# Kernel tuning notes

Measured on AMD Instinct MI355X. Metric: run time of the kernel, lower is better.

Reference implementation:

```python
import jax, jax.numpy as jnp
import numpy as np

HIDDEN = 1024
NUM_HEAD = 16
HEAD_DIM = HIDDEN // NUM_HEAD
VOCAB = 32000
MAX_LEN = 1024
EMBED = 512
BATCH = 4
SEQ = MAX_LEN  # mask broadcasting requires seq == max_len


def setup_inputs() -> dict:
    key = jax.random.key(0)
    ks = jax.random.split(key, 12)
    std = 0.02
    inp = {
        'input_ids': jax.random.randint(ks[0], (BATCH, SEQ), 0, VOCAB),
        'W_word': jax.random.normal(ks[1], (VOCAB, EMBED), jnp.float32) * std,
        'W_pos': jax.random.normal(ks[2], (MAX_LEN, EMBED), jnp.float32) * std,
        'Wq': jax.random.normal(ks[3], (HIDDEN, HIDDEN), jnp.float32) * std,
        'Wk': jax.random.normal(ks[4], (HIDDEN, HIDDEN), jnp.float32) * std,
        'Wv': jax.random.normal(ks[5], (HIDDEN, HIDDEN), jnp.float32) * std,
        'Wo': jax.random.normal(ks[6], (HIDDEN, HIDDEN), jnp.float32) * std,
        'W1': jax.random.normal(ks[7], (4 * HIDDEN, HIDDEN), jnp.float32) * std,
        'W2': jax.random.normal(ks[8], (HIDDEN, 4 * HIDDEN), jnp.float32) * std,
        'W_eh': jax.random.normal(ks[9], (HIDDEN, EMBED), jnp.float32) * std,
        'W_he': jax.random.normal(ks[10], (EMBED, HIDDEN), jnp.float32) * std,
        'W_lm': jax.random.normal(ks[11], (VOCAB, EMBED), jnp.float32) * std,
    }
    return inp


def reference(input_ids, W_word, W_pos, Wq, Wk, Wv, Wo, W1, W2, W_eh, W_he, W_lm):
    B, S = input_ids.shape
    # embeddings
    h = W_word[input_ids] + W_pos[jnp.arange(S)][None, :, :]  # [B,S,E]
    h = h @ W_eh.T  # embed -> hidden, [B,S,H]
    residual = h
    # QKV projections (Linear with weight [out,in]: y = x @ W.T)
    q = (h @ Wq.T).reshape(B, S, NUM_HEAD, HEAD_DIM).transpose(0, 2, 1, 3)
    k = (h @ Wk.T).reshape(B, S, NUM_HEAD, HEAD_DIM).transpose(0, 2, 1, 3)
    v = (h @ Wv.T).reshape(B, S, NUM_HEAD, HEAD_DIM).transpose(0, 2, 1, 3)
    # note: original scales by sqrt(hidden_size), NOT sqrt(head_dim)
    scores = jnp.einsum('bhqd,bhkd->bhqk', q, k) / jnp.sqrt(jnp.float32(HIDDEN))
    mask = jnp.tril(jnp.ones((S, S), dtype=bool))[None, None]
    scores = jnp.where(mask, scores, jnp.finfo(jnp.float32).min)
    attn = jax.nn.softmax(scores.astype(jnp.float32), axis=-1)
    out = jnp.einsum('bhqk,bhkd->bhqd', attn, v)
    out = out.transpose(0, 2, 1, 3).reshape(B, S, HIDDEN)
    h = residual + out @ Wo.T
    # MLP
    residual = h
    x = jax.nn.relu(h @ W1.T)
    h = residual + x @ W2.T
    # hidden -> embed, lm head
    h = h @ W_he.T
    logits = h @ W_lm.T  # [B,S,VOCAB]
    return logits
```

## Files before the change

kernel.cpp:

```cpp
#include <hip/hip_runtime.h>
#include <hip/hip_bf16.h>

#define HIDDEN 1024
#define NHEAD 16
#define HDIM 64
#define VOCAB 32000
#define SEQLEN 1024
#define EMBED 512
#define BATCH 4
#define ROWS (BATCH*SEQLEN)

typedef __bf16 bf16x8 __attribute__((ext_vector_type(8)));
typedef float f32x4 __attribute__((ext_vector_type(4)));
typedef unsigned short u16;

#define MFMA(a_, b_, c_) __builtin_amdgcn_mfma_f32_16x16x32_bf16(a_, b_, c_, 0, 0, 0)

#define VMCNT4 asm volatile("s_waitcnt vmcnt(4)" ::: "memory")
#define VMCNT0 asm volatile("s_waitcnt vmcnt(0)" ::: "memory")
#define LGKM0  asm volatile("s_waitcnt lgkmcnt(0)" ::: "memory")
#define CFENCE asm volatile("" ::: "memory")
#define SBAR   __builtin_amdgcn_s_barrier()
#define SCHEDB __builtin_amdgcn_sched_barrier(0)

__device__ __forceinline__ u16 f2bf(float f) {
  unsigned u = __builtin_bit_cast(unsigned, f);
  u = u + 0x7FFFu + ((u >> 16) & 1u);
  return (u16)(u >> 16);
}

#define GLDS(g_, l_) __builtin_amdgcn_global_load_lds( \
    (const __attribute__((address_space(1))) void*)(g_), \
    (__attribute__((address_space(3))) void*)(l_), 16, 0, 0)

struct Prep {
  const float* src[8]; u16* dst[8];
  const float* wlm; u16* wlm_dst;
  const int* ids; const float* wword; const float* wpos; u16* h0b;
};
__global__ void prep_kernel(Prep pp) {
  int b = blockIdx.x;
  if (b < 13312) {
    int seg, off;
    if (b < 4096)        { seg = b >> 10; off = b & 1023; }
    else if (b < 8192)   { seg = 4; off = b - 4096; }
    else if (b < 12288)  { seg = 5; off = b - 8192; }
    else if (b < 12800)  { seg = 6; off = b - 12288; }
    else                 { seg = 7; off = b - 12800; }
    size_t i = ((size_t)off * 256 + threadIdx.x) * 4;
    float4 v = *(const float4*)(pp.src[seg] + i);
    unsigned a = f2bf(v.x) | ((unsigned)f2bf(v.y) << 16);
    unsigned d = f2bf(v.z) | ((unsigned)f2bf(v.w) << 16);
    *(uint2*)(pp.dst[seg] + i) = make_uint2(a, d);
  } else if (b < 29312) {
    if (!pp.wlm_dst) return;
    int off = b - 13312;
    size_t i = ((size_t)off * 256 + threadIdx.x) * 4;
    float4 v = *(const float4*)(pp.wlm + i);
    unsigned a = f2bf(v.x) | ((unsigned)f2bf(v.y) << 16);
    unsigned d = f2bf(v.z) | ((unsigned)f2bf(v.w) << 16);
    *(uint2*)(pp.wlm_dst + i) = make_uint2(a, d);
  } else {
    int off = b - 29312;
    int row = off * 2 + (threadIdx.x >> 7);
    int e = (threadIdx.x & 127) * 4;
    int s = row & (SEQLEN - 1);
    int id = pp.ids[row];
    float4 a = *(const float4*)(pp.wword + (size_t)id * EMBED + e);
    float4 c = *(const float4*)(pp.wpos + (size_t)s * EMBED + e);
    unsigned lo = f2bf(a.x + c.x) | ((unsigned)f2bf(a.y + c.y) << 16);
    unsigned hi = f2bf(a.z + c.z) | ((unsigned)f2bf(a.w + c.w) << 16);
    *(uint2*)(pp.h0b + (size_t)row * EMBED + e) = make_uint2(lo, hi);
  }
}

template<int EPI, bool WF32, bool WB16, bool BF32, bool SWZ, bool NT = false>
__global__ __launch_bounds__(256, 2) void gemm128(
    const u16* __restrict__ A, const u16* __restrict__ Bb,
    const float* __restrict__ Bf,
    float* __restrict__ C, u16* __restrict__ Cb,
    const float* __restrict__ R, int K, int ldc)
{
  __shared__ u16 As[2][128 * 64];
  __shared__ u16 Bs[2][128 * 64];
  int tid = threadIdx.x;
  int lane = tid & 63, wave = tid >> 6;
  int wr = wave >> 1, wc = wave & 1;
  int cl = lane & 15, gp = (lane >> 4) & 3;

  int bx = blockIdx.x, by = blockIdx.y;
  if (SWZ) {
    int nwg = gridDim.x * gridDim.y;
    int flat = by * gridDim.x + bx;
    int cpx = nwg >> 3;
    int swz = (flat & 7) * cpx + (flat >> 3);
    bx = swz % gridDim.x; by = swz / gridDim.x;
  }
  int m0 = bx * 128, n0 = by * 128;

  int srow8 = lane >> 3;
  int scol = (((lane & 7) - srow8) & 7) * 8;
  int pos0 = ((gp + cl) & 7) * 8;
  int pos1 = ((gp + cl + 4) & 7) * 8;

  f32x4 acc[4][4] = {};
  int nk = K >> 6;

  #pragma unroll
  for (int i = 0; i < 4; ++i) {
    int c = i * 4 + wave;
    GLDS(A + (size_t)(m0 + c * 8 + srow8) * K + scol, &As[0][c * 512]);
  }
  if (!BF32) {
    #pragma unroll
    for (int i = 0; i < 4; ++i) {
      int c = i * 4 + wave;
      GLDS(Bb + (size_t)(n0 + c * 8 + srow8) * K + scol, &Bs[0][c * 512]);
    }
  } else {
    #pragma unroll
    for (int it = 0; it < 4; ++it) {
      int idx = it * 256 + tid;
      int row = idx >> 3, p = idx & 7;
      int gc = (p - row) & 7;
      const float* src = Bf + (size_t)(n0 + row) * K + gc * 8;
      float4 v0 = *(const float4*)src, v1 = *(const float4*)(src + 4);
      union { bf16x8 v; u16 s[8]; } u;
      u.s[0]=f2bf(v0.x); u.s[1]=f2bf(v0.y); u.s[2]=f2bf(v0.z); u.s[3]=f2bf(v0.w);
      u.s[4]=f2bf(v1.x); u.s[5]=f2bf(v1.y); u.s[6]=f2bf(v1.z); u.s[7]=f2bf(v1.w);
      *(bf16x8*)&Bs[0][row * 64 + p * 8] = u.v;
    }
  }

  for (int kt = 0; kt < nk; ++kt) {
    int buf = kt & 1;
    int kb = (kt + 1) << 6;
    bool more = kt + 1 < nk;

    if (more) {
      #pragma unroll
      for (int i = 0; i < 4; ++i) {
        int c = i * 4 + wave;
        GLDS(A + (size_t)(m0 + c * 8 + srow8) * K + kb + scol, &As[buf ^ 1][c * 512]);
      }
    }
    if (BF32) { VMCNT0; } else if (more) { VMCNT4; } else { VMCNT0; }
    SCHEDB;
    SBAR;
    CFENCE; SCHEDB;

    bf16x8 af[4][2], bfv[4][2];
    #pragma unroll
    for (int n = 0; n < 4; ++n) {
      int r = (wc * 64 + n * 16 + cl) * 64;
      bfv[n][0] = *(const bf16x8*)&Bs[buf][r + pos0];
      bfv[n][1] = *(const bf16x8*)&Bs[buf][r + pos1];
    }
    #pragma unroll
    for (int m = 0; m < 4; ++m) {
      int r = (wr * 64 + m * 16 + cl) * 64;
      af[m][0] = *(const bf16x8*)&As[buf][r + pos0];
      af[m][1] = *(const bf16x8*)&As[buf][r + pos1];
    }

    __builtin_amdgcn_s_setprio(1);
    #pragma unroll
    for (int m = 0; m < 2; ++m)
      #pragma unroll
      for (int n = 0; n < 4; ++n)
        #pragma unroll
        for (int ks = 0; ks < 2; ++ks)
          acc[m][n] = MFMA(af[m][ks], bfv[n][ks], acc[m][n]);
    __builtin_amdgcn_s_setprio(0);

    if (more) {
      if (!BF32) {
        #pragma unroll
        for (int i = 0; i < 4; ++i) {
          int c = i * 4 + wave;
          GLDS(Bb + (size_t)(n0 + c * 8 + srow8) * K + kb + scol, &Bs[buf ^ 1][c * 512]);
        }
      } else {
        #pragma unroll
        for (int it = 0; it < 4; ++it) {
          int idx = it * 256 + tid;
          int row = idx >> 3, p = idx & 7;
          int gc = (p - row) & 7;
          const float* src = Bf + (size_t)(n0 + row) * K + kb + gc * 8;
          float4 v0 = *(const float4*)src, v1 = *(const float4*)(src + 4);
          union { bf16x8 v; u16 s[8]; } u;
          u.s[0]=f2bf(v0.x); u.s[1]=f2bf(v0.y); u.s[2]=f2bf(v0.z); u.s[3]=f2bf(v0.w);
          u.s[4]=f2bf(v1.x); u.s[5]=f2bf(v1.y); u.s[6]=f2bf(v1.z); u.s[7]=f2bf(v1.w);
          *(bf16x8*)&Bs[buf ^ 1][row * 64 + p * 8] = u.v;
        }
      }
    }

    __builtin_amdgcn_s_setprio(1);
    #pragma unroll
    for (int n = 0; n < 4; ++n)
      #pragma unroll
      for (int ks = 0; ks < 2; ++ks)
        acc[2][n] = MFMA(af[2][ks], bfv[n][ks], acc[2][n]);
    __builtin_amdgcn_s_setprio(0);

    LGKM0;
    SCHEDB;
    SBAR;
    CFENCE; SCHEDB;

    __builtin_amdgcn_s_setprio(1);
    #pragma unroll
    for (int n = 0; n < 4; ++n)
      #pragma unroll
      for (int ks = 0; ks < 2; ++ks)
        acc[3][n] = MFMA(af[3][ks], bfv[n][ks], acc[3][n]);
    __builtin_amdgcn_s_setprio(0);
  }

  int r0 = gp * 4;
  #pragma unroll
  for (int m = 0; m < 4; ++m) {
    #pragma unroll
    for (int n = 0; n < 4; ++n) {
      int col = n0 + wc * 64 + n * 16 + cl;
      #pragma unroll
      for (int j = 0; j < 4; ++j) {
        int row = m0 + wr * 64 + m * 16 + r0 + j;
        float v = acc[m][n][j];
        if (EPI == 1) v += R[(size_t)row * ldc + col];
        if (EPI == 2) v = fmaxf(v, 0.f);
        if (WF32) {
          if (NT) __builtin_nontemporal_store(v, &C[(size_t)row * ldc + col]);
          else C[(size_t)row * ldc + col] = v;
        }
        if (WB16) Cb[(size_t)row * ldc + col] = f2bf(v);
      }
    }
  }
}

template<int EPI, bool WF32, bool WB16, bool SWZ, bool NT = false>
__global__ __launch_bounds__(512) void gemm256(
    const u16* __restrict__ A, const u16* __restrict__ B,
    float* __restrict__ C, u16* __restrict__ Cb,
    const float* __restrict__ R, int K, int ldc)
{
  __shared__ __align__(16) u16 smem[4][256 * 64];
  int tid = threadIdx.x;
  int lane = tid & 63, wave = tid >> 6;
  int wr = wave >> 2, wc = wave & 3;
  int cl = lane & 15, gp = (lane >> 4) & 3;

  int bx = blockIdx.x, by = blockIdx.y;
  if (SWZ) {
    int nwg = gridDim.x * gridDim.y;
    int flat = by * gridDim.x + bx;
    int cpx = nwg >> 3;
    int swz = (flat & 7) * cpx + (flat >> 3);
    bx = swz % gridDim.x; by = swz / gridDim.x;
  }
  int m0 = bx * 256, n0 = by * 256;

  int srow8 = lane >> 3;
  int scol = (((lane & 7) - srow8) & 7) * 8;
  int pos0 = ((gp + cl) & 7) * 8;
  int pos1 = ((gp + cl + 4) & 7) * 8;

  f32x4 acc[8][4] = {};
  int nk = K >> 6;

  #pragma unroll
  for (int i = 0; i < 4; ++i) {
    int c = i * 8 + wave;
    GLDS(A + (size_t)(m0 + c * 8 + srow8) * K + scol, &smem[0][c * 512]);
  }
  #pragma unroll
  for (int i = 0; i < 4; ++i) {
    int c = i * 8 + wave;
    GLDS(B + (size_t)(n0 + c * 8 + srow8) * K + scol, &smem[2][c * 512]);
  }

  for (int kt = 0; kt < nk; ++kt) {
    int buf = kt & 1;
    int kb = (kt + 1) << 6;
    bool more = kt + 1 < nk;

    if (more) {
      #pragma unroll
      for (int i = 0; i < 4; ++i) {
        int c = i * 8 + wave;
        GLDS(A + (size_t)(m0 + c * 8 + srow8) * K + kb + scol, &smem[buf ^ 1][c * 512]);
      }
      VMCNT4;
    } else {
      VMCNT0;
    }
    SCHEDB;
    SBAR;
    CFENCE; SCHEDB;

    bf16x8 af0[4][2], af1[4][2], bf0[2][2], bf1[2][2];
    #pragma unroll
    for (int n = 0; n < 2; ++n) {
      int r = (wc * 64 + n * 16 + cl) * 64;
      bf0[n][0] = *(const bf16x8*)&smem[2 + buf][r + pos0];
      bf0[n][1] = *(const bf16x8*)&smem[2 + buf][r + pos1];
    }
    #pragma unroll
    for (int m = 0; m < 4; ++m) {
      int r = (wr * 128 + m * 16 + cl) * 64;
      af0[m][0] = *(const bf16x8*)&smem[buf][r + pos0];
      af0[m][1] = *(const bf16x8*)&smem[buf][r + pos1];
    }
    #pragma unroll
    for (int n = 0; n < 2; ++n) {
      int r = (wc * 64 + (n + 2) * 16 + cl) * 64;
      bf1[n][0] = *(const bf16x8*)&smem[2 + buf][r + pos0];
      bf1[n][1] = *(const bf16x8*)&smem[2 + buf][r + pos1];
    }
    #pragma unroll
    for (int m = 0; m < 4; ++m) {
      int r = (wr * 128 + (m + 4) * 16 + cl) * 64;
      af1[m][0] = *(const bf16x8*)&smem[buf][r + pos0];
      af1[m][1] = *(const bf16x8*)&smem[buf][r + pos1];
    }

    __builtin_amdgcn_s_setprio(1);
    #pragma unroll
    for (int m = 0; m < 4; ++m)
      #pragma unroll
      for (int n = 0; n < 2; ++n)
        #pragma unroll
        for (int ks = 0; ks < 2; ++ks)
          acc[m][n] = MFMA(af0[m][ks], bf0[n][ks], acc[m][n]);
    __builtin_amdgcn_s_setprio(0);

    if (more) {
      #pragma unroll
      for (int i = 0; i < 4; ++i) {
        int c = i * 8 + wave;
        GLDS(B + (size_t)(n0 + c * 8 + srow8) * K + kb + scol, &smem[2 + (buf ^ 1)][c * 512]);
      }
    }

    __builtin_amdgcn_s_setprio(1);
    #pragma unroll
    for (int m = 0; m < 4; ++m)
      #pragma unroll
      for (int n = 0; n < 2; ++n)
        #pragma unroll
        for (int ks = 0; ks < 2; ++ks)
          acc[m][n + 2] = MFMA(af0[m][ks], bf1[n][ks], acc[m][n + 2]);
    __builtin_amdgcn_s_setprio(0);

    LGKM0;
    SCHEDB;
    SBAR;
    CFENCE; SCHEDB;

    __builtin_amdgcn_s_setprio(1);
    #pragma unroll
    for (int m = 0; m < 4; ++m)
      #pragma unroll
      for (int n = 0; n < 2; ++n)
        #pragma unroll
        for (int ks = 0; ks < 2; ++ks)
          acc[m + 4][n] = MFMA(af1[m][ks], bf0[n][ks], acc[m + 4][n]);
    #pragma unroll
    for (int m = 0; m < 4; ++m)
      #pragma unroll
      for (int n = 0; n < 2; ++n)
        #pragma unroll
        for (int ks = 0; ks < 2; ++ks)
          acc[m + 4][n + 2] = MFMA(af1[m][ks], bf1[n][ks], acc[m + 4][n + 2]);
    __builtin_amdgcn_s_setprio(0);
  }

  if (WF32 && !WB16) {
    float* Cst = (float*)&smem[0][0];
    __syncthreads();
    #pragma unroll
    for (int g = 0; g < 4; ++g) {
      if ((g >> 1) == wr) {
        #pragma unroll
        for (int k = 0; k < 4; ++k) {
          int ar = (g & 1) * 4 + k;
          int rl = ar * 16 + gp * 4 - (g & 1) * 64;
          #pragma unroll
          for (int n = 0; n < 4; ++n) {
            int col = wc * 64 + n * 16 + cl;
            #pragma unroll
            for (int j = 0; j < 4; ++j)
              Cst[(rl + j) * 260 + col] = acc[ar][n][j];
          }
        }
      }
      __syncthreads();
      #pragma unroll
      for (int p = 0; p < 8; ++p) {
        int r = p * 8 + wave;
        int c4 = lane * 4;
        int grow = m0 + g * 64 + r;
        f32x4 v = *(f32x4*)&Cst[r * 260 + c4];
        if (EPI == 1) {
          f32x4 rv = *(const f32x4*)&R[(size_t)grow * ldc + n0 + c4];
          v = v + rv;
        }
        if (EPI == 2) {
          #pragma unroll
          for (int j = 0; j < 4; ++j) v[j] = fmaxf(v[j], 0.f);
        }
        if (NT) __builtin_nontemporal_store(v, (f32x4*)&C[(size_t)grow * ldc + n0 + c4]);
        else *(f32x4*)&C[(size_t)grow * ldc + n0 + c4] = v;
      }
      __syncthreads();
    }
  } else {
    int r0 = gp * 4;
    #pragma unroll
    for (int m = 0; m < 8; ++m) {
      #pragma unroll
      for (int n = 0; n < 4; ++n) {
        int col = n0 + wc * 64 + n * 16 + cl;
        #pragma unroll
        for (int j = 0; j < 4; ++j) {
          int row = m0 + wr * 128 + m * 16 + r0 + j;
          float v = acc[m][n][j];
          if (EPI == 1) v += R[(size_t)row * ldc + col];
          if (EPI == 2) v = fmaxf(v, 0.f);
          if (WF32) C[(size_t)row * ldc + col] = v;
          if (WB16) Cb[(size_t)row * ldc + col] = f2bf(v);
        }
      }
    }
  }
}

#define LSTR 72
__global__ __launch_bounds__(256) void attn_kernel(const u16* __restrict__ qkv,
                                                   u16* __restrict__ outb) {
  __shared__ u16 Ksm[2][64 * 64];
  __shared__ u16 Vsm[2][64 * LSTR];
  __shared__ u16 Psm[64 * LSTR];
  int qb = blockIdx.x, h = blockIdx.y, b = blockIdx.z;
  int tid = threadIdx.x;
  int lane = tid & 63, wave = tid >> 6;
  int cl = lane & 15, gp = lane >> 4;
  int srow8 = lane >> 3;
  int gsrc = (((lane & 7) - srow8) & 7) * 8;

  const u16* base = qkv + (size_t)b * SEQLEN * (3 * HIDDEN);

  int qrow_a = qb * 64 + wave * 16 + cl;
  const u16* qp = base + (size_t)qrow_a * (3 * HIDDEN) + h * HDIM;
  bf16x8 qf0 = *(const bf16x8*)(qp + gp * 8);
  bf16x8 qf1 = *(const bf16x8*)(qp + 32 + gp * 8);

  ushort4 vr[4];

  auto stageK = [&](int t, int bb) {
    #pragma unroll
    for (int i = 0; i < 2; ++i) {
      int c = wave * 2 + i;
      int row = c * 8 + srow8;
      GLDS(base + (size_t)(t * 64 + row) * (3 * HIDDEN) + HIDDEN + h * HDIM + gsrc,
           &Ksm[bb][c * 512]);
    }
  };
  auto loadV = [&](int t) {
    #pragma unroll
    for (int it = 0; it < 4; ++it) {
      int idx = it * 256 + tid;
      int row = idx >> 4, c4 = (idx & 15) * 4;
      vr[it] = *(const ushort4*)(base + (size_t)(t * 64 + row) * (3 * HIDDEN) +
                                 2 * HIDDEN + h * HDIM + c4);
    }
  };
  auto writeV = [&](int bb) {
    #pragma unroll
    for (int it = 0; it < 4; ++it) {
      int idx = it * 256 + tid;
      int row = idx >> 4, c4 = (idx & 15) * 4;
      Vsm[bb][(c4 + 0) * LSTR + row] = vr[it].x;
      Vsm[bb][(c4 + 1) * LSTR + row] = vr[it].y;
      Vsm[bb][(c4 + 2) * LSTR + row] = vr[it].z;
      Vsm[bb][(c4 + 3) * LSTR + row] = vr[it].w;
    }
  };

  stageK(0, 0);
  loadV(0);
  writeV(0);
  __syncthreads();

  float mrow[4], lrow[4];
  f32x4 oacc[4] = {};
  #pragma unroll
  for (int j = 0; j < 4; ++j) { mrow[j] = -INFINITY; lrow[j] = 0.f; }

  for (int t = 0; t <= qb; ++t) {
    int buf = t & 1;
    bool more = t < qb;
    if (more) { stageK(t + 1, buf ^ 1); loadV(t + 1); }

    f32x4 sfr[4];
    __builtin_amdgcn_s_setprio(1);
    #pragma unroll
    for (int n = 0; n < 4; ++n) {
      f32x4 z = {};
      bf16x8 kf0 = *(const bf16x8*)&Ksm[buf][(n * 16 + cl) * 64 + ((gp + cl) & 7) * 8];
      bf16x8 kf1 = *(const bf16x8*)&Ksm[buf][(n * 16 + cl) * 64 + ((gp + cl + 4) & 7) * 8];
      z = MFMA(qf0, kf0, z);
      z = MFMA(qf1, kf1, z);
      sfr[n] = z;
    }
    __builtin_amdgcn_s_setprio(0);

    #pragma unroll
    for (int n = 0; n < 4; ++n)
      #pragma unroll
      for (int j = 0; j < 4; ++j) {
        int qg = qb * 64 + wave * 16 + gp * 4 + j;
        int kg = t * 64 + n * 16 + cl;
        float sv = sfr[n][j] * 0.03125f;
        sfr[n][j] = (kg <= qg) ? sv : -1e30f;
      }
    float so[4];
    #pragma unroll
    for (int j = 0; j < 4; ++j) {
      float tm = fmaxf(fmaxf(sfr[0][j], sfr[1][j]), fmaxf(sfr[2][j], sfr[3][j]));
      tm = fmaxf(tm, __shfl_xor(tm, 1));
      tm = fmaxf(tm, __shfl_xor(tm, 2));
      tm = fmaxf(tm, __shfl_xor(tm, 4));
      tm = fmaxf(tm, __shfl_xor(tm, 8));
      float mn = fmaxf(mrow[j], tm);
      so[j] = __expf(mrow[j] - mn);
      mrow[j] = mn;
      float ts = 0.f;
      #pragma unroll
      for (int n = 0; n < 4; ++n) {
        float p = __expf(sfr[n][j] - mn);
        sfr[n][j] = p;
        ts += p;
      }
      ts += __shfl_xor(ts, 1); ts += __shfl_xor(ts, 2);
      ts += __shfl_xor(ts, 4); ts += __shfl_xor(ts, 8);
      lrow[j] = lrow[j] * so[j] + ts;
    }
    #pragma unroll
    for (int n = 0; n < 4; ++n)
      #pragma unroll
      for (int j = 0; j < 4; ++j)
        oacc[n][j] *= so[j];

    if (more) writeV(buf ^ 1);

    #pragma unroll
    for (int n = 0; n < 4; ++n)
      #pragma unroll
      for (int j = 0; j < 4; ++j)
        Psm[(wave * 16 + gp * 4 + j) * LSTR + n * 16 + cl] = f2bf(sfr[n][j]);
    __builtin_amdgcn_sched_barrier(0);

    bf16x8 pa0 = *(const bf16x8*)&Psm[(wave * 16 + cl) * LSTR + gp * 8];
    bf16x8 pa1 = *(const bf16x8*)&Psm[(wave * 16 + cl) * LSTR + 32 + gp * 8];
    __builtin_amdgcn_s_setprio(1);
    #pragma unroll
    for (int n = 0; n < 4; ++n) {
      bf16x8 vb0 = *(const bf16x8*)&Vsm[buf][(n * 16 + cl) * LSTR + gp * 8];
      bf16x8 vb1 = *(const bf16x8*)&Vsm[buf][(n * 16 + cl) * LSTR + 32 + gp * 8];
      oacc[n] = MFMA(pa0, vb0, oacc[n]);
      oacc[n] = MFMA(pa1, vb1, oacc[n]);
    }
    __builtin_amdgcn_s_setprio(0);

    __syncthreads();
  }

  #pragma unroll
  for (int n = 0; n < 4; ++n)
    #pragma unroll
    for (int j = 0; j < 4; ++j) {
      int qg = qb * 64 + wave * 16 + gp * 4 + j;
      int d = n * 16 + cl;
      outb[(size_t)(b * SEQLEN + qg) * HIDDEN + h * HDIM + d] = f2bf(oacc[n][j] / lrow[j]);
    }
}

extern "C" void kernel_launch(void* const* d_in, const int* in_sizes, int n_in,
                              void* d_out, int out_size, void* d_ws, size_t ws_size,
                              hipStream_t stream) {
  const int*   ids    = (const int*)d_in[0];
  const float* W_word = (const float*)d_in[1];
  const float* W_pos  = (const float*)d_in[2];
  const float* Wq     = (const float*)d_in[3];
  const float* Wk     = (const float*)d_in[4];
  const float* Wv     = (const float*)d_in[5];
  const float* Wo     = (const float*)d_in[6];
  const float* W1     = (const float*)d_in[7];
  const float* W2     = (const float*)d_in[8];
  const float* W_eh   = (const float*)d_in[9];
  const float* W_he   = (const float*)d_in[10];
  const float* W_lm   = (const float*)d_in[11];
  float* out = (float*)d_out;
  char*  ob  = (char*)d_out;
  char*  wb  = (char*)d_ws;

  const size_t MB = 1024 * 1024;
  float* h1    = (float*)(ob + 0 * MB);
  float* h2    = (float*)(ob + 16 * MB);
  u16*   h0b   = (u16*)(ob + 32 * MB);
  u16*   h1b   = (u16*)(ob + 36 * MB);
  u16*   qkvb  = (u16*)(ob + 44 * MB);
  u16*   attnb = (u16*)(ob + 68 * MB);
  u16*   h2b   = (u16*)(ob + 76 * MB);
  u16*   xb    = (u16*)(ob + 84 * MB);
  u16*   h3b   = (u16*)(ob + 116 * MB);
  u16*   Wqkv_b= (u16*)(ob + 124 * MB);
  u16*   Wo_b  = (u16*)(ob + 130 * MB);
  u16*   W1_b  = (u16*)(ob + 132 * MB);
  u16*   W2_b  = (u16*)(ob + 140 * MB);
  u16*   Weh_b = (u16*)(ob + 148 * MB);
  u16*   Whe_b = (u16*)(ob + 149 * MB);
  u16*   he_b  = (u16*)(wb + 0);
  u16*   Wlm_b = (u16*)(wb + 4 * MB);
  bool big_ws = ws_size >= 36 * MB;

  Prep pp;
  pp.src[0] = Wq;  pp.dst[0] = Wqkv_b + 0 * 1024 * 1024;
  pp.src[1] = Wk;  pp.dst[1] = Wqkv_b + 1 * 1024 * 1024;
  pp.src[2] = Wv;  pp.dst[2] = Wqkv_b + 2 * 1024 * 1024;
  pp.src[3] = Wo;  pp.dst[3] = Wo_b;
  pp.src[4] = W1;  pp.dst[4] = W1_b;
  pp.src[5] = W2;  pp.dst[5] = W2_b;
  pp.src[6] = W_eh; pp.dst[6] = Weh_b;
  pp.src[7] = W_he; pp.dst[7] = Whe_b;
  pp.wlm = W_lm; pp.wlm_dst = big_ws ? Wlm_b : nullptr;
  pp.ids = ids; pp.wword = W_word; pp.wpos = W_pos; pp.h0b = h0b;
  prep_kernel<<<dim3(31360), 256, 0, stream>>>(pp);

  gemm128<0, true, true, false, false><<<dim3(32, 8), 256, 0, stream>>>(
      h0b, Weh_b, nullptr, h1, h1b, nullptr, 512, HIDDEN);
  gemm128<0, false, true, false, false><<<dim3(32, 24), 256, 0, stream>>>(
      h1b, Wqkv_b, nullptr, nullptr, qkvb, nullptr, 1024, 3 * HIDDEN);
  attn_kernel<<<dim3(16, 16, 4), 256, 0, stream>>>(qkvb, attnb);
  gemm128<1, true, true, false, false><<<dim3(32, 8), 256, 0, stream>>>(
      attnb, Wo_b, nullptr, h2, h2b, h1, 1024, HIDDEN);
  gemm256<2, false, true, false><<<dim3(16, 16), 512, 0, stream>>>(
      h2b, W1_b, nullptr, xb, nullptr, 1024, 4 * HIDDEN);
  gemm128<1, false, true, false, false><<<dim3(32, 8), 256, 0, stream>>>(
      xb, W2_b, nullptr, nullptr, h3b, h2, 4096, HIDDEN);
  gemm128<0, false, true, false, false><<<dim3(32, 4), 256, 0, stream>>>(
      h3b, Whe_b, nullptr, nullptr, he_b, nullptr, 1024, EMBED);
  if (big_ws)
    gemm256<0, true, false, true, true><<<dim3(16, 125), 512, 0, stream>>>(
        he_b, Wlm_b, out, nullptr, nullptr, 512, VOCAB);
  else
    gemm128<0, true, false, true, true, true><<<dim3(32, 250), 256, 0, stream>>>(
        he_b, nullptr, W_lm, out, nullptr, nullptr, 512, VOCAB);
}
```

Measured before the change: 495.3 us.

## Pair causal attention blocks, use bf16 residuals, and templatize GEMM tile width

Attention now has each workgroup handle query block i and 15-i, which evens out work under the causal mask, halves the grid, and shares K/V staging between the two blocks. Residual adds read bf16 copies instead of fp32 h1/h2, so the fp32 writes and reads of those buffers are dropped. A BN template lets the small W_he GEMM use 64-wide tiles and double its grid, and a coalesced LDS-staged epilogue is added for fp32-only outputs. Rounding the residuals to bf16 lowers precision, and the pairing raises register pressure in the attention kernel.

Result: faster. 416.0 us (-16.0%).

```diff
diff --git a/kernel.cpp b/kernel.cpp
--- a/kernel.cpp
+++ b/kernel.cpp
@@ -27,6 +27,10 @@
   unsigned u = __builtin_bit_cast(unsigned, f);
   u = u + 0x7FFFu + ((u >> 16) & 1u);
   return (u16)(u >> 16);
+}
+__device__ __forceinline__ float bf2f(u16 s) {
+  unsigned u = (unsigned)s << 16;
+  return __builtin_bit_cast(float, u);
 }
 
 #define GLDS(g_, l_) __builtin_amdgcn_global_load_lds( \
@@ -74,15 +78,21 @@
   }
 }
 
-template<int EPI, bool WF32, bool WB16, bool BF32, bool SWZ, bool NT = false>
+template<int EPI, bool WF32, bool WB16, bool BF32, bool SWZ, bool NT, int BN>
 __global__ __launch_bounds__(256, 2) void gemm128(
     const u16* __restrict__ A, const u16* __restrict__ Bb,
     const float* __restrict__ Bf,
     float* __restrict__ C, u16* __restrict__ Cb,
-    const float* __restrict__ R, int K, int ldc)
+    const u16* __restrict__ R, int K, int ldc)
 {
-  __shared__ u16 As[2][128 * 64];
-  __shared__ u16 Bs[2][128 * 64];
+  constexpr int NF  = BN / 32;
+  constexpr int BCH = BN / 32;
+  __shared__ __align__(16) u16 smem[16384 + 2 * BN * 64];
+  u16* As0 = &smem[0];
+  u16* As1 = &smem[8192];
+  u16* Bs0 = &smem[16384];
+  u16* Bs1 = &smem[16384 + BN * 64];
+
   int tid = threadIdx.x;
   int lane = tid & 63, wave = tid >> 6;
   int wr = wave >> 1, wc = wave & 1;
@@ -96,30 +106,30 @@
     int swz = (flat & 7) * cpx + (flat >> 3);
     bx = swz % gridDim.x; by = swz / gridDim.x;
   }
-  int m0 = bx * 128, n0 = by * 128;
+  int m0 = bx * 128, n0 = by * BN;
 
   int srow8 = lane >> 3;
   int scol = (((lane & 7) - srow8) & 7) * 8;
   int pos0 = ((gp + cl) & 7) * 8;
   int pos1 = ((gp + cl + 4) & 7) * 8;
 
-  f32x4 acc[4][4] = {};
+  f32x4 acc[4][NF] = {};
   int nk = K >> 6;
 
   #pragma unroll
   for (int i = 0; i < 4; ++i) {
     int c = i * 4 + wave;
-    GLDS(A + (size_t)(m0 + c * 8 + srow8) * K + scol, &As[0][c * 512]);
+    GLDS(A + (size_t)(m0 + c * 8 + srow8) * K + scol, As0 + c * 512);
   }
   if (!BF32) {
     #pragma unroll
-    for (int i = 0; i < 4; ++i) {
+    for (int i = 0; i < BCH; ++i) {
       int c = i * 4 + wave;
-      GLDS(Bb + (size_t)(n0 + c * 8 + srow8) * K + scol, &Bs[0][c * 512]);
+      GLDS(Bb + (size_t)(n0 + c * 8 + srow8) * K + scol, Bs0 + c * 512);
     }
   } else {
     #pragma unroll
-    for (int it = 0; it < 4; ++it) {
+    for (int it = 0; it < BN / 32; ++it) {
       int idx = it * 256 + tid;
       int row = idx >> 3, p = idx & 7;
       int gc = (p - row) & 7;
@@ -128,12 +138,16 @@
       union { bf16x8 v; u16 s[8]; } u;
       u.s[0]=f2bf(v0.x); u.s[1]=f2bf(v0.y); u.s[2]=f2bf(v0.z); u.s[3]=f2bf(v0.w);
       u.s[4]=f2bf(v1.x); u.s[5]=f2bf(v1.y); u.s[6]=f2bf(v1.z); u.s[7]=f2bf(v1.w);
-      *(bf16x8*)&Bs[0][row * 64 + p * 8] = u.v;
+      *(bf16x8*)&Bs0[row * 64 + p * 8] = u.v;
     }
   }
 
   for (int kt = 0; kt < nk; ++kt) {
     int buf = kt & 1;
+    u16* Asb = buf ? As1 : As0;
+    u16* Bsb = buf ? Bs1 : Bs0;
+    u16* Asn = buf ? As0 : As1;
+    u16* Bsn = buf ? Bs0 : Bs1;
     int kb = (kt + 1) << 6;
     bool more = kt + 1 < nk;
 
@@ -141,7 +155,7 @@
       #pragma unroll
       for (int i = 0; i < 4; ++i) {
         int c = i * 4 + wave;
-        GLDS(A + (size_t)(m0 + c * 8 + srow8) * K + kb + scol, &As[buf ^ 1][c * 512]);
+        GLDS(A + (size_t)(m0 + c * 8 + srow8) * K + kb + scol, Asn + c * 512);
       }
     }
     if (BF32) { VMCNT0; } else if (more) { VMCNT4; } else { VMCNT0; }
@@ -149,25 +163,25 @@
     SBAR;
     CFENCE; SCHEDB;
 
-    bf16x8 af[4][2], bfv[4][2];
-    #pragma unroll
-    for (int n = 0; n < 4; ++n) {
-      int r = (wc * 64 + n * 16 + cl) * 64;
-      bfv[n][0] = *(const bf16x8*)&Bs[buf][r + pos0];
-      bfv[n][1] = *(const bf16x8*)&Bs[buf][r + pos1];
+    bf16x8 af[4][2], bfv[NF][2];
+    #pragma unroll
+    for (int n = 0; n < NF; ++n) {
+      int r = (wc * (BN / 2) + n * 16 + cl) * 64;
+      bfv[n][0] = *(const bf16x8*)&Bsb[r + pos0];
+      bfv[n][1] = *(const bf16x8*)&Bsb[r + pos1];
     }
     #pragma unroll
     for (int m = 0; m < 4; ++m) {
       int r = (wr * 64 + m * 16 + cl) * 64;
-      af[m][0] = *(const bf16x8*)&As[buf][r + pos0];
-      af[m][1] = *(const bf16x8*)&As[buf][r + pos1];
+      af[m][0] = *(const bf16x8*)&Asb[r + pos0];
+      af[m][1] = *(const bf16x8*)&Asb[r + pos1];
     }
 
     __builtin_amdgcn_s_setprio(1);
     #pragma unroll
     for (int m = 0; m < 2; ++m)
       #pragma unroll
-      for (int n = 0; n < 4; ++n)
+      for (int n = 0; n < NF; ++n)
         #pragma unroll
         for (int ks = 0; ks < 2; ++ks)
           acc[m][n] = MFMA(af[m][ks], bfv[n][ks], acc[m][n]);
@@ -176,13 +190,13 @@
     if (more) {
       if (!BF32) {
         #pragma unroll
-        for (int i = 0; i < 4; ++i) {
+        for (int i = 0; i < BCH; ++i) {
           int c = i * 4 + wave;
-          GLDS(Bb + (size_t)(n0 + c * 8 + srow8) * K + kb + scol, &Bs[buf ^ 1][c * 512]);
+          GLDS(Bb + (size_t)(n0 + c * 8 + srow8) * K + kb + scol, Bsn + c * 512);
         }
       } else {
         #pragma unroll
-        for (int it = 0; it < 4; ++it) {
+        for (int it = 0; it < BN / 32; ++it) {
           int idx = it * 256 + tid;
           int row = idx >> 3, p = idx & 7;
           int gc = (p - row) & 7;
@@ -191,14 +205,14 @@
           union { bf16x8 v; u16 s[8]; } u;
           u.s[0]=f2bf(v0.x); u.s[1]=f2bf(v0.y); u.s[2]=f2bf(v0.z); u.s[3]=f2bf(v0.w);
           u.s[4]=f2bf(v1.x); u.s[5]=f2bf(v1.y); u.s[6]=f2bf(v1.z); u.s[7]=f2bf(v1.w);
-          *(bf16x8*)&Bs[buf ^ 1][row * 64 + p * 8] = u.v;
+          *(bf16x8*)&Bsn[row * 64 + p * 8] = u.v;
         }
       }
     }
 
     __builtin_amdgcn_s_setprio(1);
     #pragma unroll
-    for (int n = 0; n < 4; ++n)
+    for (int n = 0; n < NF; ++n)
       #pragma unroll
       for (int ks = 0; ks < 2; ++ks)
         acc[2][n] = MFMA(af[2][ks], bfv[n][ks], acc[2][n]);
@@ -211,30 +225,63 @@
 
     __builtin_amdgcn_s_setprio(1);
     #pragma unroll
-    for (int n = 0; n < 4; ++n)
+    for (int n = 0; n < NF; ++n)
       #pragma unroll
       for (int ks = 0; ks < 2; ++ks)
         acc[3][n] = MFMA(af[3][ks], bfv[n][ks], acc[3][n]);
     __builtin_amdgcn_s_setprio(0);
   }
 
-  int r0 = gp * 4;
-  #pragma unroll
-  for (int m = 0; m < 4; ++m) {
-    #pragma unroll
-    for (int n = 0; n < 4; ++n) {
-      int col = n0 + wc * 64 + n * 16 + cl;
-      #pragma unroll
-      for (int j = 0; j < 4; ++j) {
-        int row = m0 + wr * 64 + m * 16 + r0 + j;
-        float v = acc[m][n][j];
-        if (EPI == 1) v += R[(size_t)row * ldc + col];
-        if (EPI == 2) v = fmaxf(v, 0.f);
-        if (WF32) {
-          if (NT) __builtin_nontemporal_store(v, &C[(size_t)row * ldc + col]);
-          else C[(size_t)row * ldc + col] = v;
-        }
-        if (WB16) Cb[(size_t)row * ldc + col] = f2bf(v);
+  if constexpr (WF32 && !WB16 && BN == 128) {
+    float* Cst = (float*)&smem[0];
+    __syncthreads();
+    #pragma unroll
+    for (int g = 0; g < 2; ++g) {
+      if (wr == g) {
+        #pragma unroll
+        for (int m = 0; m < 4; ++m)
+          #pragma unroll
+          for (int n = 0; n < 4; ++n)
+            #pragma unroll
+            for (int j = 0; j < 4; ++j)
+              Cst[(m * 16 + gp * 4 + j) * 132 + wc * 64 + n * 16 + cl] = acc[m][n][j];
+      }
+      __syncthreads();
+      int r2 = lane >> 5, cw = lane & 31;
+      #pragma unroll
+      for (int p = 0; p < 8; ++p) {
+        int r = p * 8 + wave * 2 + r2;
+        int grow = m0 + g * 64 + r;
+        f32x4 v = *(f32x4*)&Cst[r * 132 + cw * 4];
+        if constexpr (EPI == 1) {
+          ushort4 rv = *(const ushort4*)&R[(size_t)grow * ldc + n0 + cw * 4];
+          v[0] += bf2f(rv.x); v[1] += bf2f(rv.y); v[2] += bf2f(rv.z); v[3] += bf2f(rv.w);
+        }
+        if constexpr (EPI == 2) {
+          #pragma unroll
+          for (int j = 0; j < 4; ++j) v[j] = fmaxf(v[j], 0.f);
+        }
+        if (NT) __builtin_nontemporal_store(v, (f32x4*)&C[(size_t)grow * ldc + n0 + cw * 4]);
+        else *(f32x4*)&C[(size_t)grow * ldc + n0 + cw * 4] = v;
+      }
+      __syncthreads();
+    }
+  } else {
+    int r0 = gp * 4;
+    #pragma unroll
+    for (int m = 0; m < 4; ++m) {
+      #pragma unroll
+      for (int n = 0; n < NF; ++n) {
+        int col = n0 + wc * (BN / 2) + n * 16 + cl;
+        #pragma unroll
+        for (int j = 0; j < 4; ++j) {
+          int row = m0 + wr * 64 + m * 16 + r0 + j;
+          float v = acc[m][n][j];
+          if (EPI == 1) v += bf2f(R[(size_t)row * ldc + col]);
+          if (EPI == 2) v = fmaxf(v, 0.f);
+          if (WF32) C[(size_t)row * ldc + col] = v;
+          if (WB16) Cb[(size_t)row * ldc + col] = f2bf(v);
+        }
       }
     }
   }
@@ -244,7 +291,7 @@
 __global__ __launch_bounds__(512) void gemm256(
     const u16* __restrict__ A, const u16* __restrict__ B,
     float* __restrict__ C, u16* __restrict__ Cb,
-    const float* __restrict__ R, int K, int ldc)
+    const u16* __restrict__ R, int K, int ldc)
 {
   __shared__ __align__(16) u16 smem[4][256 * 64];
   int tid = threadIdx.x;
@@ -377,7 +424,7 @@
     __builtin_amdgcn_s_setprio(0);
   }
 
-  if (WF32 && !WB16) {
+  if constexpr (WF32 && !WB16) {
     float* Cst = (float*)&smem[0][0];
     __syncthreads();
     #pragma unroll
@@ -403,11 +450,11 @@
         int c4 = lane * 4;
         int grow = m0 + g * 64 + r;
         f32x4 v = *(f32x4*)&Cst[r * 260 + c4];
-        if (EPI == 1) {
-          f32x4 rv = *(const f32x4*)&R[(size_t)grow * ldc + n0 + c4];
-          v = v + rv;
-        }
-        if (EPI == 2) {
+        if constexpr (EPI == 1) {
+          ushort4 rv = *(const ushort4*)&R[(size_t)grow * ldc + n0 + c4];
+          v[0] += bf2f(rv.x); v[1] += bf2f(rv.y); v[2] += bf2f(rv.z); v[3] += bf2f(rv.w);
+        }
+        if constexpr (EPI == 2) {
           #pragma unroll
           for (int j = 0; j < 4; ++j) v[j] = fmaxf(v[j], 0.f);
         }
@@ -427,7 +474,7 @@
         for (int j = 0; j < 4; ++j) {
           int row = m0 + wr * 128 + m * 16 + r0 + j;
           float v = acc[m][n][j];
-          if (EPI == 1) v += R[(size_t)row * ldc + col];
+          if (EPI == 1) v += bf2f(R[(size_t)row * ldc + col]);
           if (EPI == 2) v = fmaxf(v, 0.f);
           if (WF32) C[(size_t)row * ldc + col] = v;
           if (WB16) Cb[(size_t)row * ldc + col] = f2bf(v);
@@ -443,7 +490,8 @@
   __shared__ u16 Ksm[2][64 * 64];
   __shared__ u16 Vsm[2][64 * LSTR];
   __shared__ u16 Psm[64 * LSTR];
-  int qb = blockIdx.x, h = blockIdx.y, b = blockIdx.z;
+  int pi = blockIdx.x, h = blockIdx.y, b = blockIdx.z;
+  int qbA = pi, qbB = 15 - pi;
   int tid = threadIdx.x;
   int lane = tid & 63, wave = tid >> 6;
   int cl = lane & 15, gp = lane >> 4;
@@ -452,13 +500,17 @@
 
   const u16* base = qkv + (size_t)b * SEQLEN * (3 * HIDDEN);
 
-  int qrow_a = qb * 64 + wave * 16 + cl;
-  const u16* qp = base + (size_t)qrow_a * (3 * HIDDEN) + h * HDIM;
-  bf16x8 qf0 = *(const bf16x8*)(qp + gp * 8);
-  bf16x8 qf1 = *(const bf16x8*)(qp + 32 + gp * 8);
+  bf16x8 qA0, qA1, qB0, qB1;
+  {
+    const u16* qp = base + (size_t)(qbA * 64 + wave * 16 + cl) * (3 * HIDDEN) + h * HDIM;
+    qA0 = *(const bf16x8*)(qp + gp * 8);
+    qA1 = *(const bf16x8*)(qp + 32 + gp * 8);
+    const u16* qq = base + (size_t)(qbB * 64 + wave * 16 + cl) * (3 * HIDDEN) + h * HDIM;
+    qB0 = *(const bf16x8*)(qq + gp * 8);
+    qB1 = *(const bf16x8*)(qq + 32 + gp * 8);
+  }
 
   ushort4 vr[4];
-
   auto stageK = [&](int t, int bb) {
     #pragma unroll
     for (int i = 0; i < 2; ++i) {
@@ -489,21 +541,13 @@
     }
   };
 
-  stageK(0, 0);
-  loadV(0);
-  writeV(0);
-  __syncthreads();
-
-  float mrow[4], lrow[4];
-  f32x4 oacc[4] = {};
+  float mA[4], lA[4], mB[4], lB[4];
+  f32x4 oA[4] = {}, oB[4] = {};
   #pragma unroll
-  for (int j = 0; j < 4; ++j) { mrow[j] = -INFINITY; lrow[j] = 0.f; }
-
-  for (int t = 0; t <= qb; ++t) {
-    int buf = t & 1;
-    bool more = t < qb;
-    if (more) { stageK(t + 1, buf ^ 1); loadV(t + 1); }
-
+  for (int j = 0; j < 4; ++j) { mA[j] = -INFINITY; lA[j] = 0.f; mB[j] = -INFINITY; lB[j] = 0.f; }
+
+  auto stateStep = [&](int t, int buf, int qb, bf16x8 q0, bf16x8 q1,
+                       float* mrow, float* lrow, f32x4* oacc) {
     f32x4 sfr[4];
     __builtin_amdgcn_s_setprio(1);
     #pragma unroll
@@ -511,20 +555,24 @@
       f32x4 z = {};
       bf16x8 kf0 = *(const bf16x8*)&Ksm[buf][(n * 16 + cl) * 64 + ((gp + cl) & 7) * 8];
       bf16x8 kf1 = *(const bf16x8*)&Ksm[buf][(n * 16 + cl) * 64 + ((gp + cl + 4) & 7) * 8];
-      z = MFMA(qf0, kf0, z);
-      z = MFMA(qf1, kf1, z);
+      z = MFMA(q0, kf0, z);
+      z = MFMA(q1, kf1, z);
       sfr[n] = z;
     }
     __builtin_amdgcn_s_setprio(0);
 
+    bool diag = (t == qb);
     #pragma unroll
     for (int n = 0; n < 4; ++n)
       #pragma unroll
       for (int j = 0; j < 4; ++j) {
-        int qg = qb * 64 + wave * 16 + gp * 4 + j;
-        int kg = t * 64 + n * 16 + cl;
         float sv = sfr[n][j] * 0.03125f;
-        sfr[n][j] = (kg <= qg) ? sv : -1e30f;
+        if (diag) {
+          int lr = wave * 16 + gp * 4 + j;
+          int lc = n * 16 + cl;
+          sv = (lc <= lr) ? sv : -1e30f;
+        }
+        sfr[n][j] = sv;
       }
     float so[4];
     #pragma unroll
@@ -554,8 +602,6 @@
       for (int j = 0; j < 4; ++j)
         oacc[n][j] *= so[j];
 
-    if (more) writeV(buf ^ 1);
-
     #pragma unroll
     for (int n = 0; n < 4; ++n)
       #pragma unroll
@@ -574,6 +620,22 @@
       oacc[n] = MFMA(pa1, vb1, oacc[n]);
     }
     __builtin_amdgcn_s_setprio(0);
+  };
+
+  stageK(0, 0);
+  loadV(0);
+  writeV(0);
+  __syncthreads();
+
+  for (int t = 0; t <= qbB; ++t) {
+    int buf = t & 1;
+    bool more = t < qbB;
+    if (more) { stageK(t + 1, buf ^ 1); loadV(t + 1); }
+
+    stateStep(t, buf, qbB, qB0, qB1, mB, lB, oB);
+    if (more) writeV(buf ^ 1);
+    if (t <= qbA)
+      stateStep(t, buf, qbA, qA0, qA1, mA, lA, oA);
 
     __syncthreads();
   }
@@ -582,9 +644,10 @@
   for (int n = 0; n < 4; ++n)
     #pragma unroll
     for (int j = 0; j < 4; ++j) {
-      int qg = qb * 64 + wave * 16 + gp * 4 + j;
+      int lr = wave * 16 + gp * 4 + j;
       int d = n * 16 + cl;
-      outb[(size_t)(b * SEQLEN + qg) * HIDDEN + h * HDIM + d] = f2bf(oacc[n][j] / lrow[j]);
+      outb[(size_t)(b * SEQLEN + qbA * 64 + lr) * HIDDEN + h * HDIM + d] = f2bf(oA[n][j] / lA[j]);
+      outb[(size_t)(b * SEQLEN + qbB * 64 + lr) * HIDDEN + h * HDIM + d] = f2bf(oB[n][j] / lB[j]);
     }
 }
 
@@ -608,8 +671,6 @@
   char*  wb  = (char*)d_ws;
 
   const size_t MB = 1024 * 1024;
-  float* h1    = (float*)(ob + 0 * MB);
-  float* h2    = (float*)(ob + 16 * MB);
   u16*   h0b   = (u16*)(ob + 32 * MB);
   u16*   h1b   = (u16*)(ob + 36 * MB);
   u16*   qkvb  = (u16*)(ob + 44 * MB);
@@ -640,23 +701,23 @@
   pp.ids = ids; pp.wword = W_word; pp.wpos = W_pos; pp.h0b = h0b;
   prep_kernel<<<dim3(31360), 256, 0, stream>>>(pp);
 
-  gemm128<0, true, true, false, false><<<dim3(32, 8), 256, 0, stream>>>(
-      h0b, Weh_b, nullptr, h1, h1b, nullptr, 512, HIDDEN);
-  gemm128<0, false, true, false, false><<<dim3(32, 24), 256, 0, stream>>>(
+  gemm128<0, false, true, false, false, false, 128><<<dim3(32, 8), 256, 0, stream>>>(
+      h0b, Weh_b, nullptr, nullptr, h1b, nullptr, 512, HIDDEN);
+  gemm128<0, false, true, false, false, false, 128><<<dim3(32, 24), 256, 0, stream>>>(
       h1b, Wqkv_b, nullptr, nullptr, qkvb, nullptr, 1024, 3 * HIDDEN);
-  attn_kernel<<<dim3(16, 16, 4), 256, 0, stream>>>(qkvb, attnb);
-  gemm128<1, true, true, false, false><<<dim3(32, 8), 256, 0, stream>>>(
-      attnb, Wo_b, nullptr, h2, h2b, h1, 1024, HIDDEN);
+  attn_kernel<<<dim3(8, 16, 4), 256, 0, stream>>>(qkvb, attnb);
+  gemm128<1, false, true, false, false, false, 128><<<dim3(32, 8), 256, 0, stream>>>(
+      attnb, Wo_b, nullptr, nullptr, h2b, h1b, 1024, HIDDEN);
   gemm256<2, false, true, false><<<dim3(16, 16), 512, 0, stream>>>(
       h2b, W1_b, nullptr, xb, nullptr, 1024, 4 * HIDDEN);
-  gemm128<1, false, true, false, false><<<dim3(32, 8), 256, 0, stream>>>(
-      xb, W2_b, nullptr, nullptr, h3b, h2, 4096, HIDDEN);
-  gemm128<0, false, true, false, false><<<dim3(32, 4), 256, 0, stream>>>(
+  gemm128<1, false, true, false, false, false, 128><<<dim3(32, 8), 256, 0, stream>>>(
+      xb, W2_b, nullptr, nullptr, h3b, h2b, 4096, HIDDEN);
+  gemm128<0, false, true, false, false, false, 64><<<dim3(32, 8), 256, 0, stream>>>(
       h3b, Whe_b, nullptr, nullptr, he_b, nullptr, 1024, EMBED);
   if (big_ws)
     gemm256<0, true, false, true, true><<<dim3(16, 125), 512, 0, stream>>>(
         he_b, Wlm_b, out, nullptr, nullptr, 512, VOCAB);
   else
-    gemm128<0, true, false, true, true, true><<<dim3(32, 250), 256, 0, stream>>>(
+    gemm128<0, true, false, true, true, true, 128><<<dim3(32, 250), 256, 0, stream>>>(
         he_b, nullptr, W_lm, out, nullptr, nullptr, 512, VOCAB);
 }
```
